# Optimization experiments

Hardware: AMD Instinct MI355X
Metric: run time of the kernel (lower is better)

## Reference

```python
import jax, jax.numpy as jnp
import numpy as np

VAR_XY = 0.1  # SSD encoding variances
VAR_WH = 0.2


def _iou(truths, priors):
    # truths [G,4], priors [P,4] in corner form (x1,y1,x2,y2) -> [G,P]
    lt = jnp.maximum(truths[:, None, :2], priors[None, :, :2])
    rb = jnp.minimum(truths[:, None, 2:], priors[None, :, 2:])
    wh = jnp.clip(rb - lt, 0.0, None)
    inter = wh[..., 0] * wh[..., 1]
    area_t = (truths[:, 2] - truths[:, 0]) * (truths[:, 3] - truths[:, 1])
    area_p = (priors[:, 2] - priors[:, 0]) * (priors[:, 3] - priors[:, 1])
    return inter / (area_t[:, None] + area_p[None, :] - inter)


def _encode(truths, matched):
    # truths [G,1,4], matched priors [G,k,4], corner form -> SSD offsets [G,k,4]
    p_cxcy = (matched[..., :2] + matched[..., 2:]) * 0.5
    p_wh = matched[..., 2:] - matched[..., :2]
    g_cxcy = (truths[..., :2] + truths[..., 2:]) * 0.5
    g_wh = truths[..., 2:] - truths[..., :2]
    off_xy = (g_cxcy - p_cxcy) / (VAR_XY * p_wh)
    off_wh = jnp.log(g_wh / p_wh) / VAR_WH
    return jnp.concatenate([off_xy, off_wh], axis=-1)


def setup_inputs() -> dict:
    key = jax.random.key(0)
    k1, k2, k3, k4 = jax.random.split(key, 4)
    B, P, G = 16, 32768, 128
    # priors: valid corner-form boxes built from centers + sizes
    p_c = jax.random.uniform(k1, (B, P, 2), minval=0.1, maxval=0.9)
    p_s = jax.random.uniform(k2, (B, P, 2), minval=0.02, maxval=0.3)
    priors = jnp.concatenate([p_c - p_s * 0.5, p_c + p_s * 0.5], axis=-1)
    rpn_rois = jnp.stack([priors, priors], axis=1)  # [B,2,P,4]; channel 1 used
    # GT boxes, valid corner form
    t_c = jax.random.uniform(k3, (B, G, 2), minval=0.1, maxval=0.9)
    t_s = jax.random.uniform(k4, (B, G, 2), minval=0.05, maxval=0.4)
    targets = jnp.concatenate([t_c - t_s * 0.5, t_c + t_s * 0.5], axis=-1)
    return {"rpn_rois": rpn_rois, "targets": targets, "expand_num": 4}


def reference(rpn_rois, targets, expand_num):
    defaults = rpn_rois[:, 1]  # [B,P,4]

    def per_image(truths, priors):
        ious = _iou(truths, priors)                      # [G,P]
        _, idx = jax.lax.top_k(ious, expand_num)         # [G,k] best priors per GT
        matched = priors[idx]                            # [G,k,4]
        off = _encode(truths[:, None, :], matched)       # [G,k,4]
        return off.reshape(-1, 4)                        # [G*k,4]

    return jax.vmap(per_image)(targets, defaults)        # [B, G*k, 4]
```

## Files before the change

### kernel.cpp

```cpp
#include <hip/hip_runtime.h>

#define B 16
#define P 32768
#define NG 128
#define KTOP 4
#define NTB 64
#define SAMP 2048
#define CAPL 16

typedef unsigned long long u64;
typedef unsigned int u32;

__device__ __forceinline__ void ceu(u64 &x, u64 &y) {
    u64 a = x, b = y; bool gt = a > b;
    x = gt ? a : b;  y = gt ? b : a;
}
__device__ __forceinline__ void cef(float &x, float &y) {
    float h = fmaxf(x, y), l = fminf(x, y); x = h; y = l;
}

#define INS4(x, a0, a1, a2, a3)                                   \
    {                                                             \
        bool g0 = (x) > a0, g1 = (x) > a1, g2 = (x) > a2, g3 = (x) > a3; \
        u64 n3 = g2 ? a2 : (g3 ? (x) : a3);                       \
        u64 n2 = g1 ? a1 : (g2 ? (x) : a2);                       \
        u64 n1 = g0 ? a0 : (g1 ? (x) : a1);                       \
        u64 n0 = g0 ? (x) : a0;                                   \
        a0 = n0; a1 = n1; a2 = n2; a3 = n3;                       \
    }

__global__ __launch_bounds__(256)
void k_tau(const float* __restrict__ rois, const float* __restrict__ targets,
           float* __restrict__ tbl)
{
    #pragma clang fp contract(off)
    const int blk = blockIdx.x;
    const int b = blk >> 7, g = blk & (NG - 1);
    const int tid = threadIdx.x, lane = tid & 63, wv = tid >> 6;

    const float4 t = *(const float4*)(targets + ((size_t)(b * NG + g)) * 4);
    const float areaT = (t.z - t.x) * (t.w - t.y);
    const float4* __restrict__ pv = (const float4*)(rois + ((size_t)(2 * b + 1)) * P * 4);

    __shared__ float sf[4][4];
    float w0 = -1.f, w1 = -1.f, w2 = -1.f, w3 = -1.f;
    #pragma unroll
    for (int it = 0; it < SAMP / 256; ++it) {
        float4 q = pv[it * 256 + tid];
        float ap = (q.z - q.x) * (q.w - q.y);
        float ltx = fmaxf(t.x, q.x), lty = fmaxf(t.y, q.y);
        float rbx = fminf(t.z, q.z), rby = fminf(t.w, q.w);
        float wx = fmaxf(rbx - ltx, 0.0f);
        float wy = fmaxf(rby - lty, 0.0f);
        float inter = wx * wy;
        float iou = inter / ((areaT + ap) - inter);
        float x = iou, hh;
        hh = fmaxf(w0, x); x = fminf(w0, x); w0 = hh;
        hh = fmaxf(w1, x); x = fminf(w1, x); w1 = hh;
        hh = fmaxf(w2, x); x = fminf(w2, x); w2 = hh;
        w3 = fmaxf(w3, x);
    }
    #pragma unroll
    for (int d = 32; d >= 1; d >>= 1) {
        float n0 = __shfl_down(w0, d, 64);
        float n1 = __shfl_down(w1, d, 64);
        float n2 = __shfl_down(w2, d, 64);
        float n3 = __shfl_down(w3, d, 64);
        cef(w0, n3); cef(w1, n2); cef(w2, n1); cef(w3, n0);
        cef(w0, w2); cef(w1, w3); cef(w0, w1); cef(w2, w3);
    }
    if (lane == 0) { sf[wv][0] = w0; sf[wv][1] = w1; sf[wv][2] = w2; sf[wv][3] = w3; }
    __syncthreads();
    if (tid == 0) {
        float m0 = -1.f, m1 = -1.f, m2 = -1.f, m3 = -1.f;
        #pragma unroll
        for (int j = 0; j < 16; ++j) {
            float x = sf[j >> 2][j & 3], hh;
            hh = fmaxf(m0, x); x = fminf(m0, x); m0 = hh;
            hh = fmaxf(m1, x); x = fminf(m1, x); m1 = hh;
            hh = fmaxf(m2, x); x = fminf(m2, x); m2 = hh;
            m3 = fmaxf(m3, x);
        }
        float sl = (m3 / (1.0f + m3)) * (1.0f - 2e-4f);
        float* dst = tbl + (size_t)blk * 8;
        dst[0] = t.x; dst[1] = t.y; dst[2] = t.z; dst[3] = t.w;
        dst[4] = sl;  dst[5] = sl * areaT; dst[6] = areaT; dst[7] = m3;
    }
}

__global__ __launch_bounds__(256, 8)
void k_scan(const float* __restrict__ rois, const float* __restrict__ tbl,
            u64* __restrict__ part)
{
    #pragma clang fp contract(off)
    const int blk = blockIdx.x;
    const int b = blk >> 6, tile = blk & (NTB - 1);
    const int tid = threadIdx.x;
    const int p0 = (tile << 9) | tid;
    const int p1 = p0 + 256;

    __shared__ u32 lcnt[NG];
    __shared__ u64 llist[NG][CAPL];

    for (int i = tid; i < NG; i += 256) lcnt[i] = 0;

    const float4* __restrict__ pvb = (const float4*)(rois + ((size_t)(2 * b + 1)) * P * 4);
    const float4 q0 = pvb[p0];
    const float4 q1 = pvb[p1];
    const float ap0 = (q0.z - q0.x) * (q0.w - q0.y);
    const float ap1 = (q1.z - q1.x) * (q1.w - q1.y);
    const float* __restrict__ tb = tbl + (size_t)b * NG * 8;
    const u32 klo0 = (u32)(~p0), klo1 = (u32)(~p1);
    __syncthreads();

    #pragma unroll 4
    for (int g = 0; g < NG; ++g) {
        const float tt0 = tb[g * 8 + 0], tt1 = tb[g * 8 + 1];
        const float tt2 = tb[g * 8 + 2], tt3 = tb[g * 8 + 3];
        const float sl  = tb[g * 8 + 4], cA  = tb[g * 8 + 5];
        const float aT  = tb[g * 8 + 6];

        float lx0 = fmaxf(tt0, q0.x), ly0 = fmaxf(tt1, q0.y);
        float rx0 = fminf(tt2, q0.z), ry0 = fminf(tt3, q0.w);
        float wx0 = fmaxf(rx0 - lx0, 0.0f);
        float wy0 = fmaxf(ry0 - ly0, 0.0f);
        float in0 = wx0 * wy0;
        bool pa0 = in0 >= __builtin_fmaf(sl, ap0, cA);

        float lx1 = fmaxf(tt0, q1.x), ly1 = fmaxf(tt1, q1.y);
        float rx1 = fminf(tt2, q1.z), ry1 = fminf(tt3, q1.w);
        float wx1 = fmaxf(rx1 - lx1, 0.0f);
        float wy1 = fmaxf(ry1 - ly1, 0.0f);
        float in1 = wx1 * wy1;
        bool pa1 = in1 >= __builtin_fmaf(sl, ap1, cA);

        if (__builtin_expect(__any(pa0 | pa1), 0)) {
            if (pa0) {
                float sum = aT + ap0;
                float iou = in0 / (sum - in0);
                u64 key = ((u64)__float_as_uint(iou) << 32) | klo0;
                u32 slot = atomicAdd(&lcnt[g], 1u);
                if (slot < CAPL) llist[g][slot] = key;
            }
            if (pa1) {
                float sum = aT + ap1;
                float iou = in1 / (sum - in1);
                u64 key = ((u64)__float_as_uint(iou) << 32) | klo1;
                u32 slot = atomicAdd(&lcnt[g], 1u);
                if (slot < CAPL) llist[g][slot] = key;
            }
        }
    }
    __syncthreads();

    if (tid < NG) {
        const int g = tid;
        u64 f0 = 0, f1 = 0, f2 = 0, f3 = 0;
        const u32 n = lcnt[g];
        if (__builtin_expect(n > CAPL, 0)) {
            const float tt0 = tb[g * 8 + 0], tt1 = tb[g * 8 + 1];
            const float tt2 = tb[g * 8 + 2], tt3 = tb[g * 8 + 3];
            const float sl  = tb[g * 8 + 4], cA  = tb[g * 8 + 5];
            const float aT  = tb[g * 8 + 6];
            for (int i = 0; i < 512; ++i) {
                int pi = (tile << 9) | i;
                float4 qq = pvb[pi];
                float app = (qq.z - qq.x) * (qq.w - qq.y);
                float ltx = fmaxf(tt0, qq.x), lty = fmaxf(tt1, qq.y);
                float rbx = fminf(tt2, qq.z), rby = fminf(tt3, qq.w);
                float wx = fmaxf(rbx - ltx, 0.0f);
                float wy = fmaxf(rby - lty, 0.0f);
                float inter = wx * wy;
                if (inter >= __builtin_fmaf(sl, app, cA)) {
                    float sum = aT + app;
                    float iou = inter / (sum - inter);
                    u64 x = ((u64)__float_as_uint(iou) << 32) | (u32)(~pi);
                    INS4(x, f0, f1, f2, f3);
                }
            }
        } else {
            for (u32 i = 0; i < n; ++i) {
                u64 x = llist[g][i];
                INS4(x, f0, f1, f2, f3);
            }
        }
        u64* dst = part + (((size_t)b * NTB + tile) * NG + g) * KTOP;
        dst[0] = f0; dst[1] = f1; dst[2] = f2; dst[3] = f3;
    }
}

__global__ __launch_bounds__(64)
void k_top(const float* __restrict__ rois, const float* __restrict__ targets,
           const u64* __restrict__ part, float* __restrict__ out)
{
    #pragma clang fp contract(off)
    const int blk = blockIdx.x;
    const int b = blk >> 7, g = blk & (NG - 1);
    const int lane = threadIdx.x;

    const u64* __restrict__ s0 = part + (((size_t)b * NTB + lane) * NG + g) * KTOP;
    u64 a0 = s0[0], a1 = s0[1], a2 = s0[2], a3 = s0[3];
    #pragma unroll
    for (int d = 32; d >= 1; d >>= 1) {
        u64 n0 = __shfl_down(a0, d, 64);
        u64 n1 = __shfl_down(a1, d, 64);
        u64 n2 = __shfl_down(a2, d, 64);
        u64 n3 = __shfl_down(a3, d, 64);
        ceu(a0, n3); ceu(a1, n2); ceu(a2, n1); ceu(a3, n0);
        ceu(a0, a2); ceu(a1, a3); ceu(a0, a1); ceu(a2, a3);
    }
    if (lane == 0) {
        const float4 t = *(const float4*)(targets + ((size_t)(b * NG + g)) * 4);
        const float t0 = t.x, t1 = t.y, t2 = t.z, t3 = t.w;
        const float gw = t2 - t0, gh = t3 - t1;
        const float gcx = (t0 + t2) * 0.5f;
        const float gcy = (t1 + t3) * 0.5f;
        const float4* __restrict__ pv =
            (const float4*)(rois + ((size_t)(2 * b + 1)) * P * 4);
        float4* __restrict__ o4 = (float4*)out;

        u64 ks[KTOP] = {a0, a1, a2, a3};
        #pragma unroll
        for (int k = 0; k < KTOP; ++k) {
            int idx = (int)(~(u32)ks[k]) & (P - 1);
            float4 q = pv[idx];
            float pcx = (q.x + q.z) * 0.5f;
            float pcy = (q.y + q.w) * 0.5f;
            float pw  = q.z - q.x;
            float ph  = q.w - q.y;
            float4 r;
            r.x = (gcx - pcx) / (0.1f * pw);
            r.y = (gcy - pcy) / (0.1f * ph);
            r.z = logf(gw / pw) / 0.2f;
            r.w = logf(gh / ph) / 0.2f;
            o4[((size_t)(b * NG + g)) * KTOP + k] = r;
        }
    }
}

extern "C" void kernel_launch(void* const* d_in, const int* in_sizes, int n_in,
                              void* d_out, int out_size, void* d_ws, size_t ws_size,
                              hipStream_t stream) {
    const float* rois    = (const float*)d_in[0];
    const float* targets = (const float*)d_in[1];
    float* out = (float*)d_out;

    float* tbl  = (float*)d_ws;
    u64*   part = (u64*)((char*)d_ws + 65536);

    k_tau <<<dim3(B * NG),  dim3(256), 0, stream>>>(rois, targets, tbl);
    k_scan<<<dim3(B * NTB), dim3(256), 0, stream>>>(rois, tbl, part);
    k_top <<<dim3(B * NG),  dim3(64),  0, stream>>>(rois, targets, part, out);
}
```

Before: 111.4 us.

## Split GT set across two blocks per tile and defer candidate handling via bitmask

The scan kernel now launches twice as many blocks, each handling half of the ground-truth boxes for a prior tile, which doubles parallelism and halves the per-block shared memory. The threshold pass records which GTs had any passing prior in a 64-bit per-thread mask. A second loop then revisits only those GTs, reading the per-GT table from shared memory, to compute IoU and push candidates. This removes the wave-wide vote and branch from the hot loop, at the cost of recomputing the intersection for flagged GTs and reloading the prior tile in each block.

```diff
diff --git a/kernel.cpp b/kernel.cpp
--- a/kernel.cpp
+++ b/kernel.cpp
@@ -3,6 +3,7 @@
 #define B 16
 #define P 32768
 #define NG 128
+#define NGH 64
 #define KTOP 4
 #define NTB 64
 #define SAMP 2048
@@ -94,74 +95,95 @@
 {
     #pragma clang fp contract(off)
     const int blk = blockIdx.x;
-    const int b = blk >> 6, tile = blk & (NTB - 1);
+    const int b = blk >> 7;
+    const int r = blk & 127;
+    const int tile = r >> 1, gh = r & 1;
     const int tid = threadIdx.x;
     const int p0 = (tile << 9) | tid;
     const int p1 = p0 + 256;
 
-    __shared__ u32 lcnt[NG];
-    __shared__ u64 llist[NG][CAPL];
-
-    for (int i = tid; i < NG; i += 256) lcnt[i] = 0;
+    __shared__ u32   lcnt[NGH];
+    __shared__ u64   llist[NGH][CAPL];
+    __shared__ float sT[NGH * 8];
+
+    const float* __restrict__ tb = tbl + ((size_t)b * NG + (size_t)gh * NGH) * 8;
+    if (tid < NGH) lcnt[tid] = 0;
+    for (int i = tid; i < NGH * 8; i += 256) sT[i] = tb[i];
 
     const float4* __restrict__ pvb = (const float4*)(rois + ((size_t)(2 * b + 1)) * P * 4);
     const float4 q0 = pvb[p0];
     const float4 q1 = pvb[p1];
     const float ap0 = (q0.z - q0.x) * (q0.w - q0.y);
     const float ap1 = (q1.z - q1.x) * (q1.w - q1.y);
-    const float* __restrict__ tb = tbl + (size_t)b * NG * 8;
-    const u32 klo0 = (u32)(~p0), klo1 = (u32)(~p1);
     __syncthreads();
 
-    #pragma unroll 4
-    for (int g = 0; g < NG; ++g) {
+    u64 m = 0;
+    #pragma unroll 8
+    for (int g = 0; g < NGH; ++g) {
         const float tt0 = tb[g * 8 + 0], tt1 = tb[g * 8 + 1];
         const float tt2 = tb[g * 8 + 2], tt3 = tb[g * 8 + 3];
         const float sl  = tb[g * 8 + 4], cA  = tb[g * 8 + 5];
-        const float aT  = tb[g * 8 + 6];
+
+        float lx0 = fmaxf(tt0, q0.x), ly0 = fmaxf(tt1, q0.y);
+        float rx0 = fminf(tt2, q0.z), ry0 = fminf(tt3, q0.w);
+        float wx0 = fmaxf(rx0 - lx0, 0.0f);
+        float wy0 = fmaxf(ry0 - ly0, 0.0f);
+        bool pa0 = wx0 * wy0 >= __builtin_fmaf(sl, ap0, cA);
+
+        float lx1 = fmaxf(tt0, q1.x), ly1 = fmaxf(tt1, q1.y);
+        float rx1 = fminf(tt2, q1.z), ry1 = fminf(tt3, q1.w);
+        float wx1 = fmaxf(rx1 - lx1, 0.0f);
+        float wy1 = fmaxf(ry1 - ly1, 0.0f);
+        bool pa1 = wx1 * wy1 >= __builtin_fmaf(sl, ap1, cA);
+
+        m |= ((u64)(pa0 | pa1)) << g;
+    }
+
+    const u32 klo0 = (u32)(~p0), klo1 = (u32)(~p1);
+    while (m) {
+        int g = __builtin_ctzll(m);
+        m &= m - 1;
+        const float tt0 = sT[g * 8 + 0], tt1 = sT[g * 8 + 1];
+        const float tt2 = sT[g * 8 + 2], tt3 = sT[g * 8 + 3];
+        const float sl  = sT[g * 8 + 4], cA  = sT[g * 8 + 5];
+        const float aT  = sT[g * 8 + 6];
 
         float lx0 = fmaxf(tt0, q0.x), ly0 = fmaxf(tt1, q0.y);
         float rx0 = fminf(tt2, q0.z), ry0 = fminf(tt3, q0.w);
         float wx0 = fmaxf(rx0 - lx0, 0.0f);
         float wy0 = fmaxf(ry0 - ly0, 0.0f);
         float in0 = wx0 * wy0;
-        bool pa0 = in0 >= __builtin_fmaf(sl, ap0, cA);
-
+        if (in0 >= __builtin_fmaf(sl, ap0, cA)) {
+            float sum = aT + ap0;
+            float iou = in0 / (sum - in0);
+            u64 key = ((u64)__float_as_uint(iou) << 32) | klo0;
+            u32 slot = atomicAdd(&lcnt[g], 1u);
+            if (slot < CAPL) llist[g][slot] = key;
+        }
         float lx1 = fmaxf(tt0, q1.x), ly1 = fmaxf(tt1, q1.y);
         float rx1 = fminf(tt2, q1.z), ry1 = fminf(tt3, q1.w);
         float wx1 = fmaxf(rx1 - lx1, 0.0f);
         float wy1 = fmaxf(ry1 - ly1, 0.0f);
         float in1 = wx1 * wy1;
-        bool pa1 = in1 >= __builtin_fmaf(sl, ap1, cA);
-
-        if (__builtin_expect(__any(pa0 | pa1), 0)) {
-            if (pa0) {
-                float sum = aT + ap0;
-                float iou = in0 / (sum - in0);
-                u64 key = ((u64)__float_as_uint(iou) << 32) | klo0;
-                u32 slot = atomicAdd(&lcnt[g], 1u);
-                if (slot < CAPL) llist[g][slot] = key;
-            }
-            if (pa1) {
-                float sum = aT + ap1;
-                float iou = in1 / (sum - in1);
-                u64 key = ((u64)__float_as_uint(iou) << 32) | klo1;
-                u32 slot = atomicAdd(&lcnt[g], 1u);
-                if (slot < CAPL) llist[g][slot] = key;
-            }
+        if (in1 >= __builtin_fmaf(sl, ap1, cA)) {
+            float sum = aT + ap1;
+            float iou = in1 / (sum - in1);
+            u64 key = ((u64)__float_as_uint(iou) << 32) | klo1;
+            u32 slot = atomicAdd(&lcnt[g], 1u);
+            if (slot < CAPL) llist[g][slot] = key;
         }
     }
     __syncthreads();
 
-    if (tid < NG) {
+    if (tid < NGH) {
         const int g = tid;
         u64 f0 = 0, f1 = 0, f2 = 0, f3 = 0;
         const u32 n = lcnt[g];
         if (__builtin_expect(n > CAPL, 0)) {
-            const float tt0 = tb[g * 8 + 0], tt1 = tb[g * 8 + 1];
-            const float tt2 = tb[g * 8 + 2], tt3 = tb[g * 8 + 3];
-            const float sl  = tb[g * 8 + 4], cA  = tb[g * 8 + 5];
-            const float aT  = tb[g * 8 + 6];
+            const float tt0 = sT[g * 8 + 0], tt1 = sT[g * 8 + 1];
+            const float tt2 = sT[g * 8 + 2], tt3 = sT[g * 8 + 3];
+            const float sl  = sT[g * 8 + 4], cA  = sT[g * 8 + 5];
+            const float aT  = sT[g * 8 + 6];
             for (int i = 0; i < 512; ++i) {
                 int pi = (tile << 9) | i;
                 float4 qq = pvb[pi];
@@ -184,7 +206,7 @@
                 INS4(x, f0, f1, f2, f3);
             }
         }
-        u64* dst = part + (((size_t)b * NTB + tile) * NG + g) * KTOP;
+        u64* dst = part + (((size_t)b * NTB + tile) * NG + (gh * NGH + g)) * KTOP;
         dst[0] = f0; dst[1] = f1; dst[2] = f2; dst[3] = f3;
     }
 }
@@ -212,7 +234,7 @@
     if (lane == 0) {
         const float4 t = *(const float4*)(targets + ((size_t)(b * NG + g)) * 4);
         const float t0 = t.x, t1 = t.y, t2 = t.z, t3 = t.w;
-        const float gw = t2 - t0, gh = t3 - t1;
+        const float gw = t2 - t0, gh2 = t3 - t1;
         const float gcx = (t0 + t2) * 0.5f;
         const float gcy = (t1 + t3) * 0.5f;
         const float4* __restrict__ pv =
@@ -232,7 +254,7 @@
             r.x = (gcx - pcx) / (0.1f * pw);
             r.y = (gcy - pcy) / (0.1f * ph);
             r.z = logf(gw / pw) / 0.2f;
-            r.w = logf(gh / ph) / 0.2f;
+            r.w = logf(gh2 / ph) / 0.2f;
             o4[((size_t)(b * NG + g)) * KTOP + k] = r;
         }
     }
@@ -248,7 +270,7 @@
     float* tbl  = (float*)d_ws;
     u64*   part = (u64*)((char*)d_ws + 65536);
 
-    k_tau <<<dim3(B * NG),  dim3(256), 0, stream>>>(rois, targets, tbl);
-    k_scan<<<dim3(B * NTB), dim3(256), 0, stream>>>(rois, tbl, part);
-    k_top <<<dim3(B * NG),  dim3(64),  0, stream>>>(rois, targets, part, out);
-}
+    k_tau <<<dim3(B * NG),      dim3(256), 0, stream>>>(rois, targets, tbl);
+    k_scan<<<dim3(B * NTB * 2), dim3(256), 0, stream>>>(rois, tbl, part);
+    k_top <<<dim3(B * NG),      dim3(64),  0, stream>>>(rois, targets, part, out);
+}
```

New measurement: 118.4 us. +6.3%, slower.
